# Performance work log

Measured on AMD Instinct MI355X. Metric: run time of the kernel, lower is better.

## Reference

```python
import jax, jax.numpy as jnp
import numpy as np

EMB_DIM = 4096
INNER = 1024
VOCAB = 32000
NPRED = 3
B, N = 2, 512
EPS = 1e-6
# weighting constants from MLPSpeculator.__init__
STATE_W = 0.5 ** (0.5 / NPRED)
ALPHA = float(np.sqrt((1.0 - STATE_W ** 2) * (INNER / 2.0)) / STATE_W)  # emb_weight / state_weight


def _ln(x, w, b):
    # LayerNormParameterized with use_mean=False (fms default): RMS-style norm + scale + shift
    x = x * jax.lax.rsqrt(jnp.mean(x * x, axis=-1, keepdims=True) + EPS)
    return x * w + b


def setup_inputs() -> dict:
    key = jax.random.key(0)
    ks = jax.random.split(key, 8)
    s = 1.0 / np.sqrt(INNER)  # reset_parameters init scale
    return {
        "state": jax.random.normal(ks[0], (B, N, EMB_DIM), jnp.float32),
        "inds": jax.random.randint(ks[1], (B, N + NPRED), 0, VOCAB, dtype=jnp.int32),
        "emb_w": jax.random.normal(ks[2], (NPRED, VOCAB, INNER), jnp.float32) * s,
        "proj0_w": jax.random.normal(ks[3], (INNER, EMB_DIM), jnp.float32) * s,
        "proj_w": jax.random.normal(ks[4], (NPRED - 1, INNER, INNER), jnp.float32) * s,
        "head_w": jax.random.normal(ks[5], (NPRED, VOCAB, INNER), jnp.float32) * s,
        "ln_w": jnp.ones((NPRED, INNER), jnp.float32),
        "ln_b": jnp.zeros((NPRED, INNER), jnp.float32),
    }


def reference(state, inds, emb_w, proj0_w, proj_w, head_w, ln_w, ln_b):
    n = state.shape[1]
    outs = []
    for i in range(NPRED):
        z = emb_w[i][inds[:, i:i + n]]                      # [b, n, inner] gather
        W = proj0_w if i == 0 else proj_w[i - 1]            # [inner, emb_dim] or [inner, inner]
        state = jnp.einsum('bnd,id->bni', state, W)
        state = state + ALPHA * z                           # torch.add(..., alpha=emb_w/state_w)
        state = jax.nn.gelu(_ln(state, ln_w[i], ln_b[i]), approximate=False)
        outs.append(jnp.einsum('bni,vi->bnv', state, head_w[i]))  # logits [b, n, vocab]
    return jnp.stack(outs, axis=0)                          # [n_predict, b, n, vocab]
```

## Files before the change

### kernel.cpp

```cpp
#include <hip/hip_runtime.h>
#include <hip/hip_bf16.h>
#include <math.h>

#define EMB_DIM 4096
#define INNER   1024
#define VOCAB   32000
#define NPRED   3
#define SEQ     512
#define TOKENS  1024

typedef __attribute__((ext_vector_type(8))) short bf16x8;
typedef __attribute__((ext_vector_type(4))) float f32x4;

__device__ inline void gload_lds16(const void* g, void* l) {
  __builtin_amdgcn_global_load_lds(
      (const __attribute__((address_space(1))) void*)g,
      (__attribute__((address_space(3))) void*)l, 16, 0, 0);
}

__device__ inline unsigned short f2bf(float f) {
  unsigned u = __float_as_uint(f);
  u += 0x7fffu + ((u >> 16) & 1u);
  return (unsigned short)(u >> 16);
}

__global__ void cvt_kernel(const float4* __restrict__ in, ushort4* __restrict__ out, int n4) {
  int stride = gridDim.x * blockDim.x;
  for (int i = blockIdx.x * blockDim.x + threadIdx.x; i < n4; i += stride) {
    float4 v = in[i];
    ushort4 o;
    o.x = f2bf(v.x); o.y = f2bf(v.y); o.z = f2bf(v.z); o.w = f2bf(v.w);
    out[i] = o;
  }
}

__global__ __launch_bounds__(256) void proj_cvt(const __hip_bfloat16* __restrict__ A,
                                                const __hip_bfloat16* __restrict__ Bw,
                                                float* __restrict__ C, int K,
                                                const float4* __restrict__ cvsrc,
                                                ushort4* __restrict__ cvdst, int n4) {
  if (blockIdx.x >= 64) {
    for (int i = (blockIdx.x - 64) * 256 + threadIdx.x; i < n4; i += 960 * 256) {
      float4 v = cvsrc[i];
      ushort4 o;
      o.x = f2bf(v.x); o.y = f2bf(v.y); o.z = f2bf(v.z); o.w = f2bf(v.w);
      cvdst[i] = o;
    }
    return;
  }
  __shared__ char smem[16384];
  char* As = smem;
  char* Bs = smem + 8192;

  const int tid  = threadIdx.x;
  const int lane = tid & 63;
  const int wave = tid >> 6;
  const int wm = wave >> 1, wn = wave & 1;

  const int bm = (blockIdx.x >> 3) * 128;
  const int bn = (blockIdx.x & 7) * 128;
  const int N = 1024;

  const char* Ag = (const char*)(A  + (size_t)(bm + (tid >> 2)) * K + (tid & 3) * 8);
  const char* Bg = (const char*)(Bw + (size_t)(bn + (tid >> 2)) * K + (tid & 3) * 8);
  const size_t rowskip = (size_t)64 * K * 2;

  f32x4 acc[4][4] = {};

  const int fa = (wm * 64 + (lane & 15)) * 64 + (lane >> 4) * 16;
  const int fb = (wn * 64 + (lane & 15)) * 64 + (lane >> 4) * 16;

  for (int k0 = 0; k0 < K; k0 += 32) {
    gload_lds16(Ag,           As + tid * 16);
    gload_lds16(Ag + rowskip, As + 4096 + tid * 16);
    gload_lds16(Bg,           Bs + tid * 16);
    gload_lds16(Bg + rowskip, Bs + 4096 + tid * 16);
    Ag += 64; Bg += 64;
    __syncthreads();

    bf16x8 af[4], bfv[4];
#pragma unroll
    for (int m = 0; m < 4; ++m) af[m]  = *(const bf16x8*)(As + fa + m * 1024);
#pragma unroll
    for (int n = 0; n < 4; ++n) bfv[n] = *(const bf16x8*)(Bs + fb + n * 1024);
#pragma unroll
    for (int m = 0; m < 4; ++m)
#pragma unroll
      for (int n = 0; n < 4; ++n)
        acc[m][n] = __builtin_amdgcn_mfma_f32_16x16x32_bf16(af[m], bfv[n], acc[m][n], 0, 0, 0);
    __syncthreads();
  }

  const int r0 = bm + wm * 64 + (lane >> 4) * 4;
  const int c0 = bn + wn * 64 + (lane & 15);
#pragma unroll
  for (int m = 0; m < 4; ++m)
#pragma unroll
    for (int n = 0; n < 4; ++n) {
      float* Cp = C + (size_t)(r0 + m * 16) * N + (c0 + n * 16);
#pragma unroll
      for (int r = 0; r < 4; ++r)
        Cp[(size_t)r * N] = acc[m][n][r];
    }
}

__global__ __launch_bounds__(512, 2) void mega(const __hip_bfloat16* __restrict__ A,
                                               const __hip_bfloat16* __restrict__ B,
                                               float* __restrict__ C,
                                               const __hip_bfloat16* __restrict__ Pw,
                                               float* __restrict__ nsf,
                                               const float4* __restrict__ cvsrc,
                                               ushort4* __restrict__ cvdst, int n4) {
  __shared__ char smem[131072];
  const int tid  = threadIdx.x;
  const int lane = tid & 63;
  const int wave = tid >> 6;

  if (blockIdx.x >= 564) {
    for (int i = (blockIdx.x - 564) * 512 + tid; i < n4; i += 460 * 512) {
      float4 v = cvsrc[i];
      ushort4 o;
      o.x = f2bf(v.x); o.y = f2bf(v.y); o.z = f2bf(v.z); o.w = f2bf(v.w);
      cvdst[i] = o;
    }
    return;
  }

  if (blockIdx.x >= 500) {
    char* As = smem;
    char* Bs = smem + 8192;
    const int p = blockIdx.x - 500;
    const int bm = (p >> 3) * 128;
    const int bn = (p & 7) * 128;
    const int wm = wave >> 2, wn = wave & 3;

    const char* Ag = (const char*)(A  + (size_t)(bm + (tid >> 2)) * INNER + (tid & 3) * 8);
    const char* Bg = (const char*)(Pw + (size_t)(bn + (tid >> 2)) * INNER + (tid & 3) * 8);

    f32x4 acc[4][2] = {};
    const int fa = (wm * 64 + (lane & 15)) * 64 + (lane >> 4) * 16;
    const int fb = (wn * 32 + (lane & 15)) * 64 + (lane >> 4) * 16;

    for (int k0 = 0; k0 < INNER; k0 += 32) {
      gload_lds16(Ag, As + tid * 16);
      gload_lds16(Bg, Bs + tid * 16);
      Ag += 64; Bg += 64;
      __syncthreads();
      bf16x8 af[4], bfv[2];
#pragma unroll
      for (int m = 0; m < 4; ++m) af[m]  = *(const bf16x8*)(As + fa + m * 1024);
#pragma unroll
      for (int n = 0; n < 2; ++n) bfv[n] = *(const bf16x8*)(Bs + fb + n * 1024);
#pragma unroll
      for (int m = 0; m < 4; ++m)
#pragma unroll
        for (int n = 0; n < 2; ++n)
          acc[m][n] = __builtin_amdgcn_mfma_f32_16x16x32_bf16(af[m], bfv[n], acc[m][n], 0, 0, 0);
      __syncthreads();
    }
    const int r0 = bm + wm * 64 + (lane >> 4) * 4;
    const int c0 = bn + wn * 32 + (lane & 15);
#pragma unroll
    for (int m = 0; m < 4; ++m)
#pragma unroll
      for (int n = 0; n < 2; ++n) {
        float* Cp = nsf + (size_t)(r0 + m * 16) * INNER + (c0 + n * 16);
#pragma unroll
        for (int r = 0; r < 4; ++r)
          Cp[(size_t)r * INNER] = acc[m][n][r];
      }
    return;
  }

  const int M = TOKENS, N = VOCAB, K = INNER;
  const int wm = wave >> 2;
  const int wn = wave & 3;

  const int MT = M >> 8;
  const int o = blockIdx.x;
  const int q = 500 >> 3, r = 500 & 7;
  const int xcd = o & 7, idx = o >> 3;
  const int wg = (xcd < r ? xcd * (q + 1) : r * (q + 1) + (xcd - r) * q) + idx;
  const int bm = (wg % MT) * 256;
  const int bn = (wg / MT) * 256;

  f32x4 acc[8][4] = {};

  const int sl   = (lane >> 4) ^ ((lane >> 1) & 3);
  const int aoff = (wm * 128 + (lane & 15)) * 64 + sl * 16;
  const int boff = (wn * 64  + (lane & 15)) * 64 + sl * 16;

#define STAGE_T(PTR, BASEROW, LDSBASE, KT_)                                     \
  {                                                                             \
    _Pragma("unroll")                                                           \
    for (int c = 0; c < 2; ++c) {                                               \
      int chunk = c * 512 + tid;                                                \
      int row = chunk >> 2;                                                     \
      int s = (chunk & 3) ^ ((row >> 1) & 3);                                   \
      gload_lds16(PTR + (size_t)((BASEROW) + row) * K + (KT_) * 32 + s * 8,     \
                  smem + (LDSBASE) + chunk * 16);                               \
    }                                                                           \
  }

  STAGE_T(A, bm, 0,             0)
  STAGE_T(B, bn, 65536,         0)
  STAGE_T(A, bm, 16384,         1)
  STAGE_T(B, bn, 65536 + 16384, 1)
  STAGE_T(A, bm, 32768,         2)
  STAGE_T(B, bn, 65536 + 32768, 2)

  const int KT = K >> 5;
  for (int t = 0; t < KT; ++t) {
    const int bc = (t & 3) * 16384;
    const int bs = ((t + 3) & 3) * 16384;
    const char* Ab = smem + bc;
    const char* Bb = smem + 65536 + bc;

    asm volatile("s_waitcnt vmcnt(8)" ::: "memory");
    __builtin_amdgcn_s_barrier();

    const int pk = (t + 3 < KT) ? t + 3 : KT - 1;

    bf16x8 af0[4], bfv[4];
#pragma unroll
    for (int m = 0; m < 4; ++m) af0[m] = *(const bf16x8*)(Ab + aoff + m * 1024);
#pragma unroll
    for (int n = 0; n < 4; ++n) bfv[n] = *(const bf16x8*)(Bb + boff + n * 1024);
    STAGE_T(A, bm, bs, pk)
    asm volatile("s_waitcnt lgkmcnt(0)" ::: "memory");
    __builtin_amdgcn_sched_barrier(0);
    __builtin_amdgcn_s_setprio(1);
#pragma unroll
    for (int m = 0; m < 4; ++m)
#pragma unroll
      for (int n = 0; n < 4; ++n)
        acc[m][n] = __builtin_amdgcn_mfma_f32_16x16x32_bf16(af0[m], bfv[n], acc[m][n], 0, 0, 0);
    __builtin_amdgcn_s_setprio(0);

    bf16x8 af1[4];
#pragma unroll
    for (int m = 0; m < 4; ++m) af1[m] = *(const bf16x8*)(Ab + aoff + (m + 4) * 1024);
    STAGE_T(B, bn, 65536 + bs, pk)
    asm volatile("s_waitcnt lgkmcnt(0)" ::: "memory");
    __builtin_amdgcn_sched_barrier(0);
    __builtin_amdgcn_s_setprio(1);
#pragma unroll
    for (int m = 0; m < 4; ++m)
#pragma unroll
      for (int n = 0; n < 4; ++n)
        acc[m + 4][n] = __builtin_amdgcn_mfma_f32_16x16x32_bf16(af1[m], bfv[n], acc[m + 4][n], 0, 0, 0);
    __builtin_amdgcn_s_setprio(0);
    __builtin_amdgcn_sched_barrier(0);
  }
  asm volatile("s_waitcnt vmcnt(0)" ::: "memory");

  const int r0 = bm + wm * 128 + (lane >> 4) * 4;
  const int c0 = bn + wn * 64 + (lane & 15);
#pragma unroll
  for (int m = 0; m < 8; ++m)
#pragma unroll
    for (int n = 0; n < 4; ++n) {
      float* Cp = C + (size_t)(r0 + m * 16) * N + (c0 + n * 16);
#pragma unroll
      for (int rr = 0; rr < 4; ++rr)
        Cp[(size_t)rr * N] = acc[m][n][rr];
    }
#undef STAGE_T
}

__global__ __launch_bounds__(256) void fuse_ln_gelu(const float* __restrict__ ns,
    const float* __restrict__ emb,
    const int* __restrict__ inds,
    const float* __restrict__ lnw, const float* __restrict__ lnb,
    ushort4* __restrict__ out_bf16,
    int i, float alpha)
{
  const int t = blockIdx.x;
  const int b = t >> 9, n = t & 511;
  const int idx = inds[b * (SEQ + NPRED) + n + i];

  const float4* x = (const float4*)(ns + (size_t)t * INNER);
  const float4* z = (const float4*)(emb + (size_t)idx * INNER);
  const int j = threadIdx.x;

  float4 xv = x[j], zv = z[j];
  float4 v;
  v.x = xv.x + alpha * zv.x;
  v.y = xv.y + alpha * zv.y;
  v.z = xv.z + alpha * zv.z;
  v.w = xv.w + alpha * zv.w;

  float ss = v.x * v.x + v.y * v.y + v.z * v.z + v.w * v.w;
#pragma unroll
  for (int o = 32; o > 0; o >>= 1) ss += __shfl_down(ss, o);
  __shared__ float red[4];
  if ((threadIdx.x & 63) == 0) red[threadIdx.x >> 6] = ss;
  __syncthreads();
  float total = red[0] + red[1] + red[2] + red[3];
  float r = rsqrtf(total * (1.0f / INNER) + 1e-6f);

  float4 wv = ((const float4*)lnw)[j];
  float4 bv = ((const float4*)lnb)[j];
  const float inv_sqrt2 = 0.70710678118654752f;
  ushort4 o;
  float y;
  y = v.x * r * wv.x + bv.x; o.x = f2bf(0.5f * y * (1.0f + erff(y * inv_sqrt2)));
  y = v.y * r * wv.y + bv.y; o.y = f2bf(0.5f * y * (1.0f + erff(y * inv_sqrt2)));
  y = v.z * r * wv.z + bv.z; o.z = f2bf(0.5f * y * (1.0f + erff(y * inv_sqrt2)));
  y = v.w * r * wv.w + bv.w; o.w = f2bf(0.5f * y * (1.0f + erff(y * inv_sqrt2)));

  out_bf16[(size_t)t * (INNER / 4) + j] = o;
}

extern "C" void kernel_launch(void* const* d_in, const int* in_sizes, int n_in,
                              void* d_out, int out_size, void* d_ws, size_t ws_size,
                              hipStream_t stream) {
  const float* state = (const float*)d_in[0];
  const int*   inds  = (const int*)d_in[1];
  const float* emb_w = (const float*)d_in[2];
  const float* proj0 = (const float*)d_in[3];
  const float* projw = (const float*)d_in[4];
  const float* headw = (const float*)d_in[5];
  const float* lnw   = (const float*)d_in[6];
  const float* lnb   = (const float*)d_in[7];
  float* out = (float*)d_out;

  char* ws = (char*)d_ws;
  __hip_bfloat16* stateA = (__hip_bfloat16*)(ws);
  __hip_bfloat16* stateI = (__hip_bfloat16*)(ws + 8388608);
  float*          nsf    = (float*)        (ws + 10485760);
  __hip_bfloat16* p0b    = (__hip_bfloat16*)(ws + 14680064);
  __hip_bfloat16* pwb    = (__hip_bfloat16*)(ws + 23068672);
  __hip_bfloat16* hb0    = (__hip_bfloat16*)(ws + 27262976);
  __hip_bfloat16* hb1    = (__hip_bfloat16*)(ws + 92798976);

  double sw = pow(0.5, 1.0 / 6.0);
  float alpha = (float)(sqrt((1.0 - sw * sw) * (INNER / 2.0)) / sw);

  auto cvt = [&](const float* src, __hip_bfloat16* dst, size_t n) {
    int n4 = (int)(n / 4);
    int blocks = (n4 + 255) / 256;
    if (blocks > 2048) blocks = 2048;
    cvt_kernel<<<dim3(blocks), dim3(256), 0, stream>>>((const float4*)src, (ushort4*)dst, n4);
  };

  const int hn4 = (int)((size_t)VOCAB * INNER / 4);

  cvt(state, stateA, (size_t)TOKENS * EMB_DIM);
  cvt(proj0, p0b, (size_t)INNER * EMB_DIM);
  cvt(projw, pwb, (size_t)2 * INNER * INNER);

  proj_cvt<<<dim3(1024), dim3(256), 0, stream>>>(stateA, p0b, nsf, EMB_DIM,
      (const float4*)headw, (ushort4*)hb0, hn4);
  fuse_ln_gelu<<<dim3(TOKENS), dim3(256), 0, stream>>>(nsf,
      emb_w, inds, lnw, lnb, (ushort4*)stateI, 0, alpha);

  mega<<<dim3(1024), dim3(512), 0, stream>>>(stateI, hb0, out,
      pwb, nsf,
      (const float4*)(headw + (size_t)1 * VOCAB * INNER), (ushort4*)hb1, hn4);
  fuse_ln_gelu<<<dim3(TOKENS), dim3(256), 0, stream>>>(nsf,
      emb_w + (size_t)1 * VOCAB * INNER, inds,
      lnw + INNER, lnb + INNER, (ushort4*)stateI, 1, alpha);

  mega<<<dim3(1024), dim3(512), 0, stream>>>(stateI, hb1, out + (size_t)TOKENS * VOCAB,
      pwb + (size_t)INNER * INNER, nsf,
      (const float4*)(headw + (size_t)2 * VOCAB * INNER), (ushort4*)hb0, hn4);
  fuse_ln_gelu<<<dim3(TOKENS), dim3(256), 0, stream>>>(nsf,
      emb_w + (size_t)2 * VOCAB * INNER, inds,
      lnw + 2 * INNER, lnb + 2 * INNER, (ushort4*)stateI, 2, alpha);

  mega<<<dim3(500), dim3(512), 0, stream>>>(stateI, hb0, out + (size_t)2 * TOKENS * VOCAB,
      pwb, nsf, (const float4*)headw, (ushort4*)hb1, hn4);
}
```

Measured before the change: 441.5 us.

## Replace 256x256 pipelined head GEMM with simple 128x128 single-buffer tiles

The vocab-head GEMM drops its 256x256 tile, 512-thread, 4-stage LDS-pipelined path with XOR swizzle and priority hints. It uses a plain 128x128 tile with 256 threads, 16KB LDS and a load-sync-compute loop instead. The block layout also changes: 64 projection blocks first, then 460 conversion blocks, then 2000 head blocks, with a mode flag for the last launch. The smaller tiles give more blocks and occupancy, at the cost of more redundant global traffic, no prefetch overlap, and possible LDS bank conflicts.

```diff
diff --git a/kernel.cpp b/kernel.cpp
--- a/kernel.cpp
+++ b/kernel.cpp
@@ -104,160 +104,124 @@
     }
 }
 
-__global__ __launch_bounds__(512, 2) void mega(const __hip_bfloat16* __restrict__ A,
-                                               const __hip_bfloat16* __restrict__ B,
-                                               float* __restrict__ C,
-                                               const __hip_bfloat16* __restrict__ Pw,
-                                               float* __restrict__ nsf,
-                                               const float4* __restrict__ cvsrc,
-                                               ushort4* __restrict__ cvdst, int n4) {
-  __shared__ char smem[131072];
+__global__ __launch_bounds__(256) void mega(const __hip_bfloat16* __restrict__ A,
+                                            const __hip_bfloat16* __restrict__ B,
+                                            float* __restrict__ C,
+                                            const __hip_bfloat16* __restrict__ Pw,
+                                            float* __restrict__ nsf,
+                                            const float4* __restrict__ cvsrc,
+                                            ushort4* __restrict__ cvdst, int n4,
+                                            int mode) {
+  __shared__ char smem[16384];
   const int tid  = threadIdx.x;
   const int lane = tid & 63;
   const int wave = tid >> 6;
 
-  if (blockIdx.x >= 564) {
-    for (int i = (blockIdx.x - 564) * 512 + tid; i < n4; i += 460 * 512) {
-      float4 v = cvsrc[i];
-      ushort4 o;
-      o.x = f2bf(v.x); o.y = f2bf(v.y); o.z = f2bf(v.z); o.w = f2bf(v.w);
-      cvdst[i] = o;
-    }
-    return;
-  }
-
-  if (blockIdx.x >= 500) {
-    char* As = smem;
-    char* Bs = smem + 8192;
-    const int p = blockIdx.x - 500;
-    const int bm = (p >> 3) * 128;
-    const int bn = (p & 7) * 128;
-    const int wm = wave >> 2, wn = wave & 3;
-
-    const char* Ag = (const char*)(A  + (size_t)(bm + (tid >> 2)) * INNER + (tid & 3) * 8);
-    const char* Bg = (const char*)(Pw + (size_t)(bn + (tid >> 2)) * INNER + (tid & 3) * 8);
-
-    f32x4 acc[4][2] = {};
-    const int fa = (wm * 64 + (lane & 15)) * 64 + (lane >> 4) * 16;
-    const int fb = (wn * 32 + (lane & 15)) * 64 + (lane >> 4) * 16;
-
-    for (int k0 = 0; k0 < INNER; k0 += 32) {
-      gload_lds16(Ag, As + tid * 16);
-      gload_lds16(Bg, Bs + tid * 16);
-      Ag += 64; Bg += 64;
-      __syncthreads();
-      bf16x8 af[4], bfv[2];
-#pragma unroll
-      for (int m = 0; m < 4; ++m) af[m]  = *(const bf16x8*)(As + fa + m * 1024);
-#pragma unroll
-      for (int n = 0; n < 2; ++n) bfv[n] = *(const bf16x8*)(Bs + fb + n * 1024);
+  int hid;
+  if (mode == 0) {
+    if (blockIdx.x < 64) {
+      char* As = smem;
+      char* Bs = smem + 8192;
+      const int wm = wave >> 1, wn = wave & 1;
+      const int bm = (blockIdx.x >> 3) * 128;
+      const int bn = (blockIdx.x & 7) * 128;
+
+      const char* Ag = (const char*)(A  + (size_t)(bm + (tid >> 2)) * INNER + (tid & 3) * 8);
+      const char* Bg = (const char*)(Pw + (size_t)(bn + (tid >> 2)) * INNER + (tid & 3) * 8);
+      const size_t rowskip = (size_t)64 * INNER * 2;
+
+      f32x4 acc[4][4] = {};
+      const int fa = (wm * 64 + (lane & 15)) * 64 + (lane >> 4) * 16;
+      const int fb = (wn * 64 + (lane & 15)) * 64 + (lane >> 4) * 16;
+
+      for (int k0 = 0; k0 < INNER; k0 += 32) {
+        gload_lds16(Ag,           As + tid * 16);
+        gload_lds16(Ag + rowskip, As + 4096 + tid * 16);
+        gload_lds16(Bg,           Bs + tid * 16);
+        gload_lds16(Bg + rowskip, Bs + 4096 + tid * 16);
+        Ag += 64; Bg += 64;
+        __syncthreads();
+        bf16x8 af[4], bfv[4];
+#pragma unroll
+        for (int m = 0; m < 4; ++m) af[m]  = *(const bf16x8*)(As + fa + m * 1024);
+#pragma unroll
+        for (int n = 0; n < 4; ++n) bfv[n] = *(const bf16x8*)(Bs + fb + n * 1024);
+#pragma unroll
+        for (int m = 0; m < 4; ++m)
+#pragma unroll
+          for (int n = 0; n < 4; ++n)
+            acc[m][n] = __builtin_amdgcn_mfma_f32_16x16x32_bf16(af[m], bfv[n], acc[m][n], 0, 0, 0);
+        __syncthreads();
+      }
+      const int r0 = bm + wm * 64 + (lane >> 4) * 4;
+      const int c0 = bn + wn * 64 + (lane & 15);
 #pragma unroll
       for (int m = 0; m < 4; ++m)
 #pragma unroll
-        for (int n = 0; n < 2; ++n)
-          acc[m][n] = __builtin_amdgcn_mfma_f32_16x16x32_bf16(af[m], bfv[n], acc[m][n], 0, 0, 0);
-      __syncthreads();
-    }
-    const int r0 = bm + wm * 64 + (lane >> 4) * 4;
-    const int c0 = bn + wn * 32 + (lane & 15);
+        for (int n = 0; n < 4; ++n) {
+          float* Cp = nsf + (size_t)(r0 + m * 16) * INNER + (c0 + n * 16);
+#pragma unroll
+          for (int r = 0; r < 4; ++r)
+            Cp[(size_t)r * INNER] = acc[m][n][r];
+        }
+      return;
+    }
+    if (blockIdx.x < 524) {
+      for (int i = (blockIdx.x - 64) * 256 + tid; i < n4; i += 460 * 256) {
+        float4 v = cvsrc[i];
+        ushort4 o;
+        o.x = f2bf(v.x); o.y = f2bf(v.y); o.z = f2bf(v.z); o.w = f2bf(v.w);
+        cvdst[i] = o;
+      }
+      return;
+    }
+    hid = blockIdx.x - 524;
+  } else {
+    hid = blockIdx.x;
+  }
+
+  const int K = INNER, N = VOCAB;
+  const int wg = (hid & 7) * 250 + (hid >> 3);
+  const int bm = (wg & 7) * 128;
+  const int bn = (wg >> 3) * 128;
+
+  char* As = smem;
+  char* Bs = smem + 8192;
+  const int wm = wave >> 1, wn = wave & 1;
+
+  const char* Ag = (const char*)(A + (size_t)(bm + (tid >> 2)) * K + (tid & 3) * 8);
+  const char* Bg = (const char*)(B + (size_t)(bn + (tid >> 2)) * K + (tid & 3) * 8);
+  const size_t rowskip = (size_t)64 * K * 2;
+
+  f32x4 acc[4][4] = {};
+  const int fa = (wm * 64 + (lane & 15)) * 64 + (lane >> 4) * 16;
+  const int fb = (wn * 64 + (lane & 15)) * 64 + (lane >> 4) * 16;
+
+  for (int k0 = 0; k0 < K; k0 += 32) {
+    gload_lds16(Ag,           As + tid * 16);
+    gload_lds16(Ag + rowskip, As + 4096 + tid * 16);
+    gload_lds16(Bg,           Bs + tid * 16);
+    gload_lds16(Bg + rowskip, Bs + 4096 + tid * 16);
+    Ag += 64; Bg += 64;
+    __syncthreads();
+
+    bf16x8 af[4], bfv[4];
+#pragma unroll
+    for (int m = 0; m < 4; ++m) af[m]  = *(const bf16x8*)(As + fa + m * 1024);
+#pragma unroll
+    for (int n = 0; n < 4; ++n) bfv[n] = *(const bf16x8*)(Bs + fb + n * 1024);
 #pragma unroll
     for (int m = 0; m < 4; ++m)
 #pragma unroll
-      for (int n = 0; n < 2; ++n) {
-        float* Cp = nsf + (size_t)(r0 + m * 16) * INNER + (c0 + n * 16);
-#pragma unroll
-        for (int r = 0; r < 4; ++r)
-          Cp[(size_t)r * INNER] = acc[m][n][r];
-      }
-    return;
-  }
-
-  const int M = TOKENS, N = VOCAB, K = INNER;
-  const int wm = wave >> 2;
-  const int wn = wave & 3;
-
-  const int MT = M >> 8;
-  const int o = blockIdx.x;
-  const int q = 500 >> 3, r = 500 & 7;
-  const int xcd = o & 7, idx = o >> 3;
-  const int wg = (xcd < r ? xcd * (q + 1) : r * (q + 1) + (xcd - r) * q) + idx;
-  const int bm = (wg % MT) * 256;
-  const int bn = (wg / MT) * 256;
-
-  f32x4 acc[8][4] = {};
-
-  const int sl   = (lane >> 4) ^ ((lane >> 1) & 3);
-  const int aoff = (wm * 128 + (lane & 15)) * 64 + sl * 16;
-  const int boff = (wn * 64  + (lane & 15)) * 64 + sl * 16;
-
-#define STAGE_T(PTR, BASEROW, LDSBASE, KT_)                                     \
-  {                                                                             \
-    _Pragma("unroll")                                                           \
-    for (int c = 0; c < 2; ++c) {                                               \
-      int chunk = c * 512 + tid;                                                \
-      int row = chunk >> 2;                                                     \
-      int s = (chunk & 3) ^ ((row >> 1) & 3);                                   \
-      gload_lds16(PTR + (size_t)((BASEROW) + row) * K + (KT_) * 32 + s * 8,     \
-                  smem + (LDSBASE) + chunk * 16);                               \
-    }                                                                           \
-  }
-
-  STAGE_T(A, bm, 0,             0)
-  STAGE_T(B, bn, 65536,         0)
-  STAGE_T(A, bm, 16384,         1)
-  STAGE_T(B, bn, 65536 + 16384, 1)
-  STAGE_T(A, bm, 32768,         2)
-  STAGE_T(B, bn, 65536 + 32768, 2)
-
-  const int KT = K >> 5;
-  for (int t = 0; t < KT; ++t) {
-    const int bc = (t & 3) * 16384;
-    const int bs = ((t + 3) & 3) * 16384;
-    const char* Ab = smem + bc;
-    const char* Bb = smem + 65536 + bc;
-
-    asm volatile("s_waitcnt vmcnt(8)" ::: "memory");
-    __builtin_amdgcn_s_barrier();
-
-    const int pk = (t + 3 < KT) ? t + 3 : KT - 1;
-
-    bf16x8 af0[4], bfv[4];
-#pragma unroll
-    for (int m = 0; m < 4; ++m) af0[m] = *(const bf16x8*)(Ab + aoff + m * 1024);
-#pragma unroll
-    for (int n = 0; n < 4; ++n) bfv[n] = *(const bf16x8*)(Bb + boff + n * 1024);
-    STAGE_T(A, bm, bs, pk)
-    asm volatile("s_waitcnt lgkmcnt(0)" ::: "memory");
-    __builtin_amdgcn_sched_barrier(0);
-    __builtin_amdgcn_s_setprio(1);
-#pragma unroll
-    for (int m = 0; m < 4; ++m)
-#pragma unroll
       for (int n = 0; n < 4; ++n)
-        acc[m][n] = __builtin_amdgcn_mfma_f32_16x16x32_bf16(af0[m], bfv[n], acc[m][n], 0, 0, 0);
-    __builtin_amdgcn_s_setprio(0);
-
-    bf16x8 af1[4];
-#pragma unroll
-    for (int m = 0; m < 4; ++m) af1[m] = *(const bf16x8*)(Ab + aoff + (m + 4) * 1024);
-    STAGE_T(B, bn, 65536 + bs, pk)
-    asm volatile("s_waitcnt lgkmcnt(0)" ::: "memory");
-    __builtin_amdgcn_sched_barrier(0);
-    __builtin_amdgcn_s_setprio(1);
-#pragma unroll
-    for (int m = 0; m < 4; ++m)
-#pragma unroll
-      for (int n = 0; n < 4; ++n)
-        acc[m + 4][n] = __builtin_amdgcn_mfma_f32_16x16x32_bf16(af1[m], bfv[n], acc[m + 4][n], 0, 0, 0);
-    __builtin_amdgcn_s_setprio(0);
-    __builtin_amdgcn_sched_barrier(0);
-  }
-  asm volatile("s_waitcnt vmcnt(0)" ::: "memory");
-
-  const int r0 = bm + wm * 128 + (lane >> 4) * 4;
+        acc[m][n] = __builtin_amdgcn_mfma_f32_16x16x32_bf16(af[m], bfv[n], acc[m][n], 0, 0, 0);
+    __syncthreads();
+  }
+
+  const int r0 = bm + wm * 64 + (lane >> 4) * 4;
   const int c0 = bn + wn * 64 + (lane & 15);
 #pragma unroll
-  for (int m = 0; m < 8; ++m)
+  for (int m = 0; m < 4; ++m)
 #pragma unroll
     for (int n = 0; n < 4; ++n) {
       float* Cp = C + (size_t)(r0 + m * 16) * N + (c0 + n * 16);
@@ -265,7 +229,6 @@
       for (int rr = 0; rr < 4; ++rr)
         Cp[(size_t)rr * N] = acc[m][n][rr];
     }
-#undef STAGE_T
 }
 
 __global__ __launch_bounds__(256) void fuse_ln_gelu(const float* __restrict__ ns,
@@ -355,20 +318,20 @@
   fuse_ln_gelu<<<dim3(TOKENS), dim3(256), 0, stream>>>(nsf,
       emb_w, inds, lnw, lnb, (ushort4*)stateI, 0, alpha);
 
-  mega<<<dim3(1024), dim3(512), 0, stream>>>(stateI, hb0, out,
+  mega<<<dim3(2524), dim3(256), 0, stream>>>(stateI, hb0, out,
       pwb, nsf,
-      (const float4*)(headw + (size_t)1 * VOCAB * INNER), (ushort4*)hb1, hn4);
+      (const float4*)(headw + (size_t)1 * VOCAB * INNER), (ushort4*)hb1, hn4, 0);
   fuse_ln_gelu<<<dim3(TOKENS), dim3(256), 0, stream>>>(nsf,
       emb_w + (size_t)1 * VOCAB * INNER, inds,
       lnw + INNER, lnb + INNER, (ushort4*)stateI, 1, alpha);
 
-  mega<<<dim3(1024), dim3(512), 0, stream>>>(stateI, hb1, out + (size_t)TOKENS * VOCAB,
+  mega<<<dim3(2524), dim3(256), 0, stream>>>(stateI, hb1, out + (size_t)TOKENS * VOCAB,
       pwb + (size_t)INNER * INNER, nsf,
-      (const float4*)(headw + (size_t)2 * VOCAB * INNER), (ushort4*)hb0, hn4);
+      (const float4*)(headw + (size_t)2 * VOCAB * INNER), (ushort4*)hb0, hn4, 0);
   fuse_ln_gelu<<<dim3(TOKENS), dim3(256), 0, stream>>>(nsf,
       emb_w + (size_t)2 * VOCAB * INNER, inds,
       lnw + 2 * INNER, lnb + 2 * INNER, (ushort4*)stateI, 2, alpha);
 
-  mega<<<dim3(500), dim3(512), 0, stream>>>(stateI, hb0, out + (size_t)2 * TOKENS * VOCAB,
-      pwb, nsf, (const float4*)headw, (ushort4*)hb1, hn4);
-}
+  mega<<<dim3(2000), dim3(256), 0, stream>>>(stateI, hb0, out + (size_t)2 * TOKENS * VOCAB,
+      pwb, nsf, (const float4*)headw, (ushort4*)hb1, hn4, 1);
+}
```

New measurement: 608.9 us. 1.38x slower.
